# Kernel tuning notes

Hardware: AMD Instinct MI355X
Metric: run time of the kernel (lower is better)

The kernel has to match this reference:

```python
import jax, jax.numpy as jnp
import numpy as np
from jax import lax

HEADS = 4
SR = 4
LN_EPS = 1e-5


def setup_inputs() -> dict:
    key = jax.random.key(0)
    ks = jax.random.split(key, 8)
    B, N, C = 8, 4096, 256
    w_scale = 0.05  # keep attention logits in a sane range
    return {
        "x": jax.random.normal(ks[0], (B, N, C), jnp.float32),
        "h": 64,
        "w": 64,
        "Wq": jax.random.normal(ks[1], (C, C), jnp.float32) * w_scale,
        "Wkv": jax.random.normal(ks[2], (C, 2 * C), jnp.float32) * w_scale,
        "sr_w": jax.random.normal(ks[3], (C, C, SR, SR), jnp.float32) * w_scale,
        "sr_b": jnp.zeros((C,), jnp.float32),
        "ln_g": jnp.ones((C,), jnp.float32),
        "ln_b": jnp.zeros((C,), jnp.float32),
        "Wo": jax.random.normal(ks[4], (C, C), jnp.float32) * w_scale,
        "bo": jnp.zeros((C,), jnp.float32),
    }


def _layernorm(x, g, b):
    mu = x.mean(-1, keepdims=True)
    var = ((x - mu) ** 2).mean(-1, keepdims=True)
    return (x - mu) * lax.rsqrt(var + LN_EPS) * g + b


def reference(x, h, w, Wq, Wkv, sr_w, sr_b, ln_g, ln_b, Wo, bo):
    B, N, C = x.shape
    hd = C // HEADS
    scale = hd ** -0.5
    # Q projection -> [B, H, N, hd]
    q = (x @ Wq).reshape(B, N, HEADS, hd).transpose(0, 2, 1, 3)
    # spatial reduction of K/V tokens: strided conv + LayerNorm
    x_kv = x.transpose(0, 2, 1).reshape(B, C, h, w)  # b (h w) c -> b c h w
    x_kv = lax.conv_general_dilated(
        x_kv, sr_w, window_strides=(SR, SR), padding="VALID",
        dimension_numbers=("NCHW", "OIHW", "NCHW"))
    x_kv = x_kv + sr_b[None, :, None, None]
    Nk = (h // SR) * (w // SR)
    x_kv = x_kv.reshape(B, C, Nk).transpose(0, 2, 1)  # b c h w -> b (h w) c
    x_kv = _layernorm(x_kv, ln_g, ln_b)
    # KV projection -> k, v each [B, H, Nk, hd]
    kv = (x_kv @ Wkv).reshape(B, Nk, 2, HEADS, hd)
    k = kv[:, :, 0].transpose(0, 2, 1, 3)
    v = kv[:, :, 1].transpose(0, 2, 1, 3)
    # attention: full [B, H, N, Nk] score matrix, softmax over kv axis
    att = jax.nn.softmax(jnp.einsum("bhxd,bhyd->bhxy", q, k) * scale, axis=-1)
    out = jnp.einsum("bhxy,bhyd->bhxd", att, v)
    out = out.transpose(0, 2, 1, 3).reshape(B, N, C)  # b h l d -> b l (h d)
    return out @ Wo + bo
```

## Files before the change

kernel.cpp:

```cpp
#include <hip/hip_runtime.h>

typedef __bf16 bf16;
typedef bf16 bf16x8 __attribute__((ext_vector_type(8)));
typedef bf16 bf16x4 __attribute__((ext_vector_type(4)));
typedef float f32x4 __attribute__((ext_vector_type(4)));

#define MFMA16(a, b, c) __builtin_amdgcn_mfma_f32_16x16x32_bf16(a, b, c, 0, 0, 0)


__global__ void k_cvt(const float* __restrict__ in, bf16* __restrict__ out) {
  int i = (blockIdx.x * 256 + threadIdx.x) * 4;
  float4 v = *(const float4*)(in + i);
  bf16x4 o;
  o[0] = (bf16)v.x; o[1] = (bf16)v.y; o[2] = (bf16)v.z; o[3] = (bf16)v.w;
  *(bf16x4*)(out + i) = o;
}

__global__ void k_tr256(const float* __restrict__ in, bf16* __restrict__ out, int Cc) {
  int id = blockIdx.x * 256 + threadIdx.x;
  int c = id >> 8, r = id & 255;
  out[id] = (bf16)in[r * Cc + c];
}

__global__ void k_srw(const float* __restrict__ in, bf16* __restrict__ out) {
  int id = blockIdx.x * 256 + threadIdx.x;
  int o = id >> 12, rem = id & 4095;
  int i = rem >> 4, p = rem & 15;
  out[(o << 12) + (p << 8) + i] = (bf16)in[id];
}

template <int AMODE, int EMODE>
__global__ __launch_bounds__(256, 2) void k_gemm(
    const bf16* __restrict__ A, const bf16* __restrict__ Bt,
    void* __restrict__ Cout, const float* __restrict__ bias,
    int M, int N, int K) {
  constexpr int LDT = 72;
  __shared__ alignas(16) bf16 As[64 * LDT];
  __shared__ alignas(16) bf16 Bs[64 * LDT];
  int tid = threadIdx.x;
  int m0 = blockIdx.x * 64, n0 = blockIdx.y * 64;
  int kbeg = blockIdx.z * K;
  int wave = tid >> 6, lane = tid & 63;
  int quad = lane >> 4, l16 = lane & 15;

  f32x4 acc[4];
#pragma unroll
  for (int i = 0; i < 4; i++) acc[i] = (f32x4){0.f, 0.f, 0.f, 0.f};

  for (int k0 = kbeg; k0 < kbeg + K; k0 += 64) {
#pragma unroll
    for (int t = 0; t < 2; t++) {
      int c = tid + t * 256;
      int row = c >> 3, c8 = (c & 7) * 8;
      const bf16* asrc;
      if constexpr (AMODE == 0) {
        asrc = A + (size_t)(m0 + row) * K + k0 + c8;
      } else {
        int m = m0 + row;
        int b = m >> 8, tt = m & 255;
        int oh = tt >> 4, ow = tt & 15;
        int p = k0 >> 8;
        int kh = p >> 2, kw = p & 3;
        int tok = (oh * 4 + kh) * 64 + ow * 4 + kw;
        asrc = A + ((size_t)(b * 4096 + tok) << 8) + (k0 & 255) + c8;
      }
      *(bf16x8*)&As[row * LDT + c8] = *(const bf16x8*)asrc;
      *(bf16x8*)&Bs[row * LDT + c8] =
          *(const bf16x8*)(Bt + (size_t)(n0 + row) * ((AMODE == 1) ? 4096 : K) + k0 + c8);
    }
    __syncthreads();
#pragma unroll
    for (int kk = 0; kk < 64; kk += 32) {
      bf16x8 af = *(const bf16x8*)&As[(wave * 16 + l16) * LDT + kk + quad * 8];
#pragma unroll
      for (int nt = 0; nt < 4; nt++) {
        bf16x8 bfr = *(const bf16x8*)&Bs[(nt * 16 + l16) * LDT + kk + quad * 8];
        acc[nt] = MFMA16(af, bfr, acc[nt]);
      }
    }
    __syncthreads();
  }

  int rbase = m0 + wave * 16 + quad * 4;
#pragma unroll
  for (int nt = 0; nt < 4; nt++) {
    int col = n0 + nt * 16 + l16;
#pragma unroll
    for (int r = 0; r < 4; r++) {
      float v = acc[nt][r];
      int row = rbase + r;
      if constexpr (EMODE == 0) {
        ((bf16*)Cout)[(size_t)row * N + col] = (bf16)v;
      } else if constexpr (EMODE == 2) {
        int b = row >> 8, key = row & 255;
        int isv = col >> 8, c2 = col & 255;
        int hh = c2 >> 6, d = c2 & 63;
        int bh = b * 4 + hh;
        bf16* dst = (bf16*)Cout;
        if (isv == 0)
          dst[(((size_t)bh) * 256 + key) * 64 + d] = (bf16)v;
        else
          dst[32 * 256 * 64 + (((size_t)bh) * 64 + d) * 256 + key] = (bf16)v;
      } else if constexpr (EMODE == 3) {
        ((float*)Cout)[(size_t)row * N + col] = v + bias[col];
      } else {
        ((float*)Cout)[((size_t)blockIdx.z * M + row) * N + col] = v;
      }
    }
  }
}

__global__ void k_ln(const float* __restrict__ part, const float* __restrict__ srb,
                     const float* __restrict__ g, const float* __restrict__ bb,
                     bf16* __restrict__ out) {
  int row = blockIdx.x * 4 + (threadIdx.x >> 6);
  int lane = threadIdx.x & 63;
  size_t off = (size_t)row * 256 + lane * 4;
  float4 v = *(const float4*)&part[off];
#pragma unroll
  for (int z = 1; z < 8; z++) {
    float4 p = *(const float4*)&part[(size_t)z * 2048 * 256 + off];
    v.x += p.x; v.y += p.y; v.z += p.z; v.w += p.w;
  }
  int c = lane * 4;
  v.x += srb[c + 0]; v.y += srb[c + 1]; v.z += srb[c + 2]; v.w += srb[c + 3];
  float s = v.x + v.y + v.z + v.w;
#pragma unroll
  for (int i = 1; i < 64; i <<= 1) s += __shfl_xor(s, i, 64);
  float mu = s * (1.f / 256.f);
  float d0 = v.x - mu, d1 = v.y - mu, d2 = v.z - mu, d3 = v.w - mu;
  float q = d0 * d0 + d1 * d1 + d2 * d2 + d3 * d3;
#pragma unroll
  for (int i = 1; i < 64; i <<= 1) q += __shfl_xor(q, i, 64);
  float rs = rsqrtf(q * (1.f / 256.f) + 1e-5f);
  bf16x4 o;
  o[0] = (bf16)(d0 * rs * g[c + 0] + bb[c + 0]);
  o[1] = (bf16)(d1 * rs * g[c + 1] + bb[c + 1]);
  o[2] = (bf16)(d2 * rs * g[c + 2] + bb[c + 2]);
  o[3] = (bf16)(d3 * rs * g[c + 3] + bb[c + 3]);
  *(bf16x4*)&out[(size_t)row * 256 + c] = o;
}

__global__ __launch_bounds__(256, 2) void k_attn(
    const bf16* __restrict__ Q,
    const bf16* __restrict__ Kb,
    const bf16* __restrict__ Vt_g,
    bf16* __restrict__ O) {
  int bh = blockIdx.x, qt = blockIdx.y;
  int b = bh >> 2, h = bh & 3;
  int tid = threadIdx.x, wave = tid >> 6, lane = tid & 63;
  int quad = lane >> 4, l16 = lane & 15;

  __shared__ alignas(16) bf16 smem[64 * 72 + 256 * 72 + 64 * 264];
  bf16* Qs = smem;
  bf16* Ks = smem + 64 * 72;
  bf16* Vt = smem + 64 * 72 + 256 * 72;
  bf16* Ps = smem;

#pragma unroll
  for (int t = 0; t < 2; t++) {
    int c = tid + t * 256;
    int row = c >> 3, c8 = (c & 7) * 8;
    *(bf16x8*)&Qs[row * 72 + c8] =
        *(const bf16x8*)&Q[((size_t)(b * 4096 + qt * 64 + row) << 8) + h * 64 + c8];
  }
  const bf16* Kbh = Kb + (size_t)bh * 256 * 64;
#pragma unroll
  for (int t = 0; t < 8; t++) {
    int c = tid + t * 256;
    int row = c >> 3, c8 = (c & 7) * 8;
    *(bf16x8*)&Ks[row * 72 + c8] = *(const bf16x8*)&Kbh[row * 64 + c8];
  }
  const bf16* Vbh = Vt_g + (size_t)bh * 64 * 256;
#pragma unroll
  for (int t = 0; t < 8; t++) {
    int c = tid + t * 256;
    int row = c >> 5, c8 = (c & 31) * 8;
    *(bf16x8*)&Vt[row * 264 + c8] = *(const bf16x8*)&Vbh[row * 256 + c8];
  }
  __syncthreads();

  f32x4 s[16];
#pragma unroll
  for (int i = 0; i < 16; i++) s[i] = (f32x4){0.f, 0.f, 0.f, 0.f};
  bf16x8 aq0 = *(const bf16x8*)&Qs[(wave * 16 + l16) * 72 + 0 + quad * 8];
  bf16x8 aq1 = *(const bf16x8*)&Qs[(wave * 16 + l16) * 72 + 32 + quad * 8];
#pragma unroll
  for (int nt = 0; nt < 16; nt++) {
    bf16x8 b0 = *(const bf16x8*)&Ks[(nt * 16 + l16) * 72 + 0 + quad * 8];
    bf16x8 b1 = *(const bf16x8*)&Ks[(nt * 16 + l16) * 72 + 32 + quad * 8];
    s[nt] = MFMA16(aq0, b0, s[nt]);
    s[nt] = MFMA16(aq1, b1, s[nt]);
  }

  const float scale = 0.125f;
#pragma unroll
  for (int r = 0; r < 4; r++) {
    float m = -1e30f;
#pragma unroll
    for (int nt = 0; nt < 16; nt++) m = fmaxf(m, s[nt][r]);
#pragma unroll
    for (int i = 1; i < 16; i <<= 1) m = fmaxf(m, __shfl_xor(m, i, 64));
    float sum = 0.f;
#pragma unroll
    for (int nt = 0; nt < 16; nt++) {
      float e = __expf((s[nt][r] - m) * scale);
      s[nt][r] = e;
      sum += e;
    }
#pragma unroll
    for (int i = 1; i < 16; i <<= 1) sum += __shfl_xor(sum, i, 64);
    float inv = 1.f / sum;
#pragma unroll
    for (int nt = 0; nt < 16; nt++) s[nt][r] *= inv;
  }

  __syncthreads();
#pragma unroll
  for (int nt = 0; nt < 16; nt++)
#pragma unroll
    for (int r = 0; r < 4; r++)
      Ps[(wave * 16 + quad * 4 + r) * 264 + nt * 16 + l16] = (bf16)s[nt][r];
  __syncthreads();

  f32x4 o[4];
#pragma unroll
  for (int i = 0; i < 4; i++) o[i] = (f32x4){0.f, 0.f, 0.f, 0.f};
#pragma unroll
  for (int k0 = 0; k0 < 256; k0 += 32) {
    bf16x8 ap = *(const bf16x8*)&Ps[(wave * 16 + l16) * 264 + k0 + quad * 8];
#pragma unroll
    for (int nt = 0; nt < 4; nt++) {
      bf16x8 bv = *(const bf16x8*)&Vt[(nt * 16 + l16) * 264 + k0 + quad * 8];
      o[nt] = MFMA16(ap, bv, o[nt]);
    }
  }

  size_t orow = (size_t)b * 4096 + qt * 64 + wave * 16 + quad * 4;
#pragma unroll
  for (int nt = 0; nt < 4; nt++) {
    int col = h * 64 + nt * 16 + l16;
#pragma unroll
    for (int r = 0; r < 4; r++) O[(orow + r) * 256 + col] = (bf16)o[nt][r];
  }
}

extern "C" void kernel_launch(void* const* d_in, const int* in_sizes, int n_in,
                              void* d_out, int out_size, void* d_ws, size_t ws_size,
                              hipStream_t stream) {
  (void)in_sizes; (void)n_in; (void)out_size; (void)ws_size;
  const float* x   = (const float*)d_in[0];
  const float* Wq  = (const float*)d_in[3];
  const float* Wkv = (const float*)d_in[4];
  const float* srw = (const float*)d_in[5];
  const float* srb = (const float*)d_in[6];
  const float* lng = (const float*)d_in[7];
  const float* lnb = (const float*)d_in[8];
  const float* Wo  = (const float*)d_in[9];
  const float* bo  = (const float*)d_in[10];
  float* out = (float*)d_out;

  char* ws = (char*)d_ws;
  bf16*  x_bf  = (bf16*)(ws + 0);
  bf16*  Qbuf  = (bf16*)(ws + 16777216);
  bf16*  AObuf = (bf16*)(ws + 33554432);
  float* convp = (float*)(ws + 33554432);
  bf16*  WqT   = (bf16*)(ws + 50331648);
  bf16*  WkvT  = (bf16*)(ws + 50462720);
  bf16*  WoT   = (bf16*)(ws + 50724864);
  bf16*  srwT  = (bf16*)(ws + 50855936);
  bf16*  xln   = (bf16*)(ws + 55050240);
  bf16*  kvbuf = (bf16*)(ws + 56098816);

  k_cvt<<<8192, 256, 0, stream>>>(x, x_bf);
  k_tr256<<<256, 256, 0, stream>>>(Wq, WqT, 256);
  k_tr256<<<512, 256, 0, stream>>>(Wkv, WkvT, 512);
  k_tr256<<<256, 256, 0, stream>>>(Wo, WoT, 256);
  k_srw<<<4096, 256, 0, stream>>>(srw, srwT);

  k_gemm<0, 0><<<dim3(512, 4), 256, 0, stream>>>(x_bf, WqT, Qbuf, nullptr, 32768, 256, 256);
  k_gemm<1, 4><<<dim3(32, 4, 8), 256, 0, stream>>>(x_bf, srwT, convp, nullptr, 2048, 256, 512);
  k_ln<<<512, 256, 0, stream>>>(convp, srb, lng, lnb, xln);
  k_gemm<0, 2><<<dim3(32, 8), 256, 0, stream>>>(xln, WkvT, kvbuf, nullptr, 2048, 512, 256);
  k_attn<<<dim3(32, 64), 256, 0, stream>>>(Qbuf, kvbuf, kvbuf + (size_t)32 * 256 * 64, AObuf);
  k_gemm<0, 3><<<dim3(512, 4), 256, 0, stream>>>(AObuf, WoT, out, bo, 32768, 256, 256);
}
```

Before: 202.0 us.

## Fuse Q projection into attention kernel and merge prep kernels into one launch

Attention blocks now compute their Q tile directly from bf16 x and the transposed Wq in shared memory, eliminating the separate Q GEMM and the Q buffer round trip. The five conversion/transpose prep kernels are merged into a single launch with vectorized srw loads. This trades reduced launches and intermediate traffic for each x tile being re-read once per head and higher LDS usage per block, which may affect occupancy.

New measurement: 186.8 us. 7.5% less time.

```diff
diff --git a/kernel.cpp b/kernel.cpp
--- a/kernel.cpp
+++ b/kernel.cpp
@@ -7,26 +7,43 @@
 
 #define MFMA16(a, b, c) __builtin_amdgcn_mfma_f32_16x16x32_bf16(a, b, c, 0, 0, 0)
 
-
-__global__ void k_cvt(const float* __restrict__ in, bf16* __restrict__ out) {
-  int i = (blockIdx.x * 256 + threadIdx.x) * 4;
-  float4 v = *(const float4*)(in + i);
-  bf16x4 o;
-  o[0] = (bf16)v.x; o[1] = (bf16)v.y; o[2] = (bf16)v.z; o[3] = (bf16)v.w;
-  *(bf16x4*)(out + i) = o;
-}
-
-__global__ void k_tr256(const float* __restrict__ in, bf16* __restrict__ out, int Cc) {
-  int id = blockIdx.x * 256 + threadIdx.x;
-  int c = id >> 8, r = id & 255;
-  out[id] = (bf16)in[r * Cc + c];
-}
-
-__global__ void k_srw(const float* __restrict__ in, bf16* __restrict__ out) {
-  int id = blockIdx.x * 256 + threadIdx.x;
-  int o = id >> 12, rem = id & 4095;
-  int i = rem >> 4, p = rem & 15;
-  out[(o << 12) + (p << 8) + i] = (bf16)in[id];
+__global__ void k_prep(const float* __restrict__ x, const float* __restrict__ Wq,
+                       const float* __restrict__ Wkv, const float* __restrict__ Wo,
+                       const float* __restrict__ srw,
+                       bf16* __restrict__ x_bf, bf16* __restrict__ WqT,
+                       bf16* __restrict__ WkvT, bf16* __restrict__ WoT,
+                       bf16* __restrict__ srwT) {
+  int bid = blockIdx.x, tid = threadIdx.x;
+  if (bid < 8192) {
+    int i = (bid * 256 + tid) * 4;
+    float4 v = *(const float4*)(x + i);
+    bf16x4 o;
+    o[0] = (bf16)v.x; o[1] = (bf16)v.y; o[2] = (bf16)v.z; o[3] = (bf16)v.w;
+    *(bf16x4*)(x_bf + i) = o;
+  } else if (bid < 9216) {
+    int id = (bid - 8192) * 256 + tid;
+    if (id < 65536) {
+      int c = id >> 8, r = id & 255;
+      WqT[id] = (bf16)Wq[r * 256 + c];
+    } else if (id < 196608) {
+      int l = id - 65536;
+      int c = l >> 8, r = l & 255;
+      WkvT[l] = (bf16)Wkv[r * 512 + c];
+    } else {
+      int l = id - 196608;
+      int c = l >> 8, r = l & 255;
+      WoT[l] = (bf16)Wo[r * 256 + c];
+    }
+  } else {
+    int id4 = ((bid - 9216) * 256 + tid) * 4;
+    int o = id4 >> 12, rem = id4 & 4095;
+    int i = rem >> 4, p = rem & 15;
+    float4 v = *(const float4*)(srw + id4);
+    srwT[(o << 12) + ((p + 0) << 8) + i] = (bf16)v.x;
+    srwT[(o << 12) + ((p + 1) << 8) + i] = (bf16)v.y;
+    srwT[(o << 12) + ((p + 2) << 8) + i] = (bf16)v.z;
+    srwT[(o << 12) + ((p + 3) << 8) + i] = (bf16)v.w;
+  }
 }
 
 template <int AMODE, int EMODE>
@@ -89,9 +106,7 @@
     for (int r = 0; r < 4; r++) {
       float v = acc[nt][r];
       int row = rbase + r;
-      if constexpr (EMODE == 0) {
-        ((bf16*)Cout)[(size_t)row * N + col] = (bf16)v;
-      } else if constexpr (EMODE == 2) {
+      if constexpr (EMODE == 2) {
         int b = row >> 8, key = row & 255;
         int isv = col >> 8, c2 = col & 255;
         int hh = c2 >> 6, d = c2 & 63;
@@ -142,7 +157,8 @@
 }
 
 __global__ __launch_bounds__(256, 2) void k_attn(
-    const bf16* __restrict__ Q,
+    const bf16* __restrict__ xbf,
+    const bf16* __restrict__ WqT,
     const bf16* __restrict__ Kb,
     const bf16* __restrict__ Vt_g,
     bf16* __restrict__ O) {
@@ -151,32 +167,55 @@
   int tid = threadIdx.x, wave = tid >> 6, lane = tid & 63;
   int quad = lane >> 4, l16 = lane & 15;
 
-  __shared__ alignas(16) bf16 smem[64 * 72 + 256 * 72 + 64 * 264];
-  bf16* Qs = smem;
-  bf16* Ks = smem + 64 * 72;
-  bf16* Vt = smem + 64 * 72 + 256 * 72;
-  bf16* Ps = smem;
-
-#pragma unroll
-  for (int t = 0; t < 2; t++) {
+  __shared__ alignas(16) bf16 smem[39936];
+  bf16* R1 = smem;
+  bf16* R2 = smem + 18432;
+  bf16* Qs = smem + 35328;
+
+#pragma unroll
+  for (int t = 0; t < 8; t++) {
     int c = tid + t * 256;
-    int row = c >> 3, c8 = (c & 7) * 8;
-    *(bf16x8*)&Qs[row * 72 + c8] =
-        *(const bf16x8*)&Q[((size_t)(b * 4096 + qt * 64 + row) << 8) + h * 64 + c8];
-  }
+    int row = c >> 5, c8 = (c & 31) * 8;
+    *(bf16x8*)&R1[row * 264 + c8] =
+        *(const bf16x8*)&xbf[((size_t)(b * 4096 + qt * 64 + row) << 8) + c8];
+    *(bf16x8*)&R2[row * 264 + c8] =
+        *(const bf16x8*)&WqT[((size_t)(h * 64 + row) << 8) + c8];
+  }
+  __syncthreads();
+
+  f32x4 q[4];
+#pragma unroll
+  for (int i = 0; i < 4; i++) q[i] = (f32x4){0.f, 0.f, 0.f, 0.f};
+#pragma unroll
+  for (int k0 = 0; k0 < 256; k0 += 32) {
+    bf16x8 ax = *(const bf16x8*)&R1[(wave * 16 + l16) * 264 + k0 + quad * 8];
+#pragma unroll
+    for (int nt = 0; nt < 4; nt++) {
+      bf16x8 bw = *(const bf16x8*)&R2[(nt * 16 + l16) * 264 + k0 + quad * 8];
+      q[nt] = MFMA16(ax, bw, q[nt]);
+    }
+  }
+  __syncthreads();
+
+#pragma unroll
+  for (int nt = 0; nt < 4; nt++)
+#pragma unroll
+    for (int r = 0; r < 4; r++)
+      Qs[(wave * 16 + quad * 4 + r) * 72 + nt * 16 + l16] = (bf16)q[nt][r];
+
   const bf16* Kbh = Kb + (size_t)bh * 256 * 64;
 #pragma unroll
   for (int t = 0; t < 8; t++) {
     int c = tid + t * 256;
     int row = c >> 3, c8 = (c & 7) * 8;
-    *(bf16x8*)&Ks[row * 72 + c8] = *(const bf16x8*)&Kbh[row * 64 + c8];
+    *(bf16x8*)&R1[row * 72 + c8] = *(const bf16x8*)&Kbh[row * 64 + c8];
   }
   const bf16* Vbh = Vt_g + (size_t)bh * 64 * 256;
 #pragma unroll
   for (int t = 0; t < 8; t++) {
     int c = tid + t * 256;
     int row = c >> 5, c8 = (c & 31) * 8;
-    *(bf16x8*)&Vt[row * 264 + c8] = *(const bf16x8*)&Vbh[row * 256 + c8];
+    *(bf16x8*)&R2[row * 264 + c8] = *(const bf16x8*)&Vbh[row * 256 + c8];
   }
   __syncthreads();
 
@@ -187,8 +226,8 @@
   bf16x8 aq1 = *(const bf16x8*)&Qs[(wave * 16 + l16) * 72 + 32 + quad * 8];
 #pragma unroll
   for (int nt = 0; nt < 16; nt++) {
-    bf16x8 b0 = *(const bf16x8*)&Ks[(nt * 16 + l16) * 72 + 0 + quad * 8];
-    bf16x8 b1 = *(const bf16x8*)&Ks[(nt * 16 + l16) * 72 + 32 + quad * 8];
+    bf16x8 b0 = *(const bf16x8*)&R1[(nt * 16 + l16) * 72 + 0 + quad * 8];
+    bf16x8 b1 = *(const bf16x8*)&R1[(nt * 16 + l16) * 72 + 32 + quad * 8];
     s[nt] = MFMA16(aq0, b0, s[nt]);
     s[nt] = MFMA16(aq1, b1, s[nt]);
   }
@@ -220,7 +259,7 @@
   for (int nt = 0; nt < 16; nt++)
 #pragma unroll
     for (int r = 0; r < 4; r++)
-      Ps[(wave * 16 + quad * 4 + r) * 264 + nt * 16 + l16] = (bf16)s[nt][r];
+      R1[(wave * 16 + quad * 4 + r) * 264 + nt * 16 + l16] = (bf16)s[nt][r];
   __syncthreads();
 
   f32x4 o[4];
@@ -228,10 +267,10 @@
   for (int i = 0; i < 4; i++) o[i] = (f32x4){0.f, 0.f, 0.f, 0.f};
 #pragma unroll
   for (int k0 = 0; k0 < 256; k0 += 32) {
-    bf16x8 ap = *(const bf16x8*)&Ps[(wave * 16 + l16) * 264 + k0 + quad * 8];
+    bf16x8 ap = *(const bf16x8*)&R1[(wave * 16 + l16) * 264 + k0 + quad * 8];
 #pragma unroll
     for (int nt = 0; nt < 4; nt++) {
-      bf16x8 bv = *(const bf16x8*)&Vt[(nt * 16 + l16) * 264 + k0 + quad * 8];
+      bf16x8 bv = *(const bf16x8*)&R2[(nt * 16 + l16) * 264 + k0 + quad * 8];
       o[nt] = MFMA16(ap, bv, o[nt]);
     }
   }
@@ -262,26 +301,19 @@
 
   char* ws = (char*)d_ws;
   bf16*  x_bf  = (bf16*)(ws + 0);
-  bf16*  Qbuf  = (bf16*)(ws + 16777216);
-  bf16*  AObuf = (bf16*)(ws + 33554432);
+  bf16*  AObuf = (bf16*)(ws + 16777216);
   float* convp = (float*)(ws + 33554432);
   bf16*  WqT   = (bf16*)(ws + 50331648);
   bf16*  WkvT  = (bf16*)(ws + 50462720);
   bf16*  WoT   = (bf16*)(ws + 50724864);
   bf16*  srwT  = (bf16*)(ws + 50855936);
-  bf16*  xln   = (bf16*)(ws + 55050240);
-  bf16*  kvbuf = (bf16*)(ws + 56098816);
-
-  k_cvt<<<8192, 256, 0, stream>>>(x, x_bf);
-  k_tr256<<<256, 256, 0, stream>>>(Wq, WqT, 256);
-  k_tr256<<<512, 256, 0, stream>>>(Wkv, WkvT, 512);
-  k_tr256<<<256, 256, 0, stream>>>(Wo, WoT, 256);
-  k_srw<<<4096, 256, 0, stream>>>(srw, srwT);
-
-  k_gemm<0, 0><<<dim3(512, 4), 256, 0, stream>>>(x_bf, WqT, Qbuf, nullptr, 32768, 256, 256);
+  bf16*  xln   = (bf16*)(ws + 52953088);
+  bf16*  kvbuf = (bf16*)(ws + 54001664);
+
+  k_prep<<<10240, 256, 0, stream>>>(x, Wq, Wkv, Wo, srw, x_bf, WqT, WkvT, WoT, srwT);
   k_gemm<1, 4><<<dim3(32, 4, 8), 256, 0, stream>>>(x_bf, srwT, convp, nullptr, 2048, 256, 512);
   k_ln<<<512, 256, 0, stream>>>(convp, srb, lng, lnb, xln);
   k_gemm<0, 2><<<dim3(32, 8), 256, 0, stream>>>(xln, WkvT, kvbuf, nullptr, 2048, 512, 256);
-  k_attn<<<dim3(32, 64), 256, 0, stream>>>(Qbuf, kvbuf, kvbuf + (size_t)32 * 256 * 64, AObuf);
+  k_attn<<<dim3(32, 64), 256, 0, stream>>>(x_bf, WqT, kvbuf, kvbuf + (size_t)32 * 256 * 64, AObuf);
   k_gemm<0, 3><<<dim3(512, 4), 256, 0, stream>>>(AObuf, WoT, out, bo, 32768, 256, 256);
 }
```
